# Kernel optimization log

Hardware: AMD Instinct MI355X
Metric: run time of the kernel (lower is better)

## Reference

```python
import jax, jax.numpy as jnp
import numpy as np

B, M, T, D, V = 16, 4096, 4, 256, 40000
HOPS, NLAYER, CONV_MAX = 3, 3, 512
PAD = 1  # PAD_token: embedding row zeroed (padding_idx)


def setup_inputs() -> dict:
    key = jax.random.key(0)
    ks = jax.random.split(key, 10)
    story = jax.random.randint(ks[0], (B, M, T), 0, V)
    conv_len = jax.random.randint(ks[1], (B,), 1, CONV_MAX)
    kb_len = jax.random.randint(ks[2], (B,), 0, M - CONV_MAX)
    query = jax.random.normal(ks[3], (B, 1, D), jnp.float32)
    history_outputs = jax.random.normal(ks[4], (B, CONV_MAX, D), jnp.float32)
    query_vector = jax.random.normal(ks[5], (B, D), jnp.float32)
    global_pointer = jax.random.uniform(ks[6], (B, M), jnp.float32)
    # hop+1 embedding tables, N(0, 0.1), padding row zeroed
    C_emb = jax.random.normal(ks[7], (HOPS + 1, V, D), jnp.float32) * 0.1
    C_emb = C_emb.at[:, PAD, :].set(0.0)
    Tg_w = jax.random.normal(ks[8], (HOPS + 1, D, D), jnp.float32) * 0.05
    Tg_b = jnp.zeros((HOPS + 1, D), jnp.float32)
    FW_w = jax.random.normal(ks[9], (D, D), jnp.float32) * 0.05
    FW_b = jnp.zeros((D,), jnp.float32)
    return dict(story=story, kb_len=kb_len, conv_len=conv_len, query=query,
                history_outputs=history_outputs, query_vector=query_vector,
                global_pointer=global_pointer, C_emb=C_emb, Tg_w=Tg_w,
                Tg_b=Tg_b, FW_w=FW_w, FW_b=FW_b)


def _add_lm(mem, kb_len, conv_len, hist):
    # mem: [B,M,D]; add hist[b, 0:conv_len[b]] into mem[b, kb_len[b]:kb_len[b]+conv_len[b]]
    j = jnp.arange(mem.shape[1])[None, :]                       # [1,M]
    start = kb_len[:, None]
    mask = (j >= start) & (j < start + conv_len[:, None])       # [B,M]
    idx = jnp.clip(j - start, 0, hist.shape[1] - 1)             # [B,M]
    gathered = jnp.take_along_axis(hist, idx[..., None], axis=1)  # [B,M,D]
    return mem + jnp.where(mask[..., None], gathered, 0.0)


def _embed(table, story, kb_len, conv_len, hist):
    # bag-of-words over the mem-token axis, then LM-embedding add
    e = jnp.sum(table[story], axis=2)                           # [B,M,D]
    return _add_lm(e, kb_len, conv_len, hist)


def reference(story, kb_len, conv_len, query, history_outputs, query_vector,
              global_pointer, C_emb, Tg_w, Tg_b, FW_w, FW_b):
    # ---- load_memory (eval mode: dropout is identity; ablationH/G = False) ----
    q = query[:, 0, :]                                          # [B,D]
    last_u = None
    m_story = None
    for layer in range(NLAYER):
        iq = q
        if layer > 0:
            g = jax.nn.sigmoid(iq @ Tg_w[0].T + Tg_b[0])
            iq = last_u[0] * g + iq * (1.0 - g)
        u = [iq]
        m_story = []
        embC = None
        for hop in range(HOPS):
            embA = _embed(C_emb[hop], story, kb_len, conv_len, history_outputs)
            logit = jnp.einsum('bmd,bd->bm', embA, u[-1])
            prob = jax.nn.softmax(logit, axis=1)
            embC = _embed(C_emb[hop + 1], story, kb_len, conv_len, history_outputs)
            o_k = jnp.einsum('bm,bmd->bd', prob, embC)
            u_k = u[-1] + o_k
            if layer > 0:
                g = jax.nn.sigmoid(u_k @ Tg_w[hop + 1].T + Tg_b[hop + 1])
                u_k = last_u[hop + 1] * g + u_k * (1.0 - g)
            u.append(u_k)
            m_story.append(embA)
        m_story.append(embC)
        last_u = u
        q = jax.nn.relu(u[-1] @ FW_w.T + FW_b)
    # ---- forward (decoder-side read over last layer's memories) ----
    uf = query_vector
    psoft = None
    logits = None
    for hop in range(HOPS):
        mA = m_story[hop] * global_pointer[:, :, None]
        logits = jnp.einsum('bmd,bd->bm', mA, uf)
        psoft = jax.nn.softmax(logits, axis=1)
        mC = m_story[hop + 1] * global_pointer[:, :, None]
        uf = uf + jnp.einsum('bm,bmd->bd', psoft, mC)
    return (psoft, logits, uf, m_story[-1])
```

## Files before the change

kernel.cpp:

```cpp
#include <hip/hip_runtime.h>
#include <math.h>

#define Bdim 16
#define Mdim 4096
#define Tdim 4
#define Ddim 256
#define Vdim 40000
#define CONVMAX 512

__global__ void embed_kernel(const int* __restrict__ story, const int* __restrict__ kb_len,
                             const int* __restrict__ conv_len, const float* __restrict__ hist,
                             const float* __restrict__ C_emb, const float* __restrict__ qv,
                             const float* __restrict__ gp,
                             float* __restrict__ e1, float* __restrict__ e2,
                             float* __restrict__ e3, float* __restrict__ logits0) {
    int bid = blockIdx.x;
    int k   = bid / (Bdim * (Mdim / 4));
    int rem = bid % (Bdim * (Mdim / 4));
    int b   = rem / (Mdim / 4);
    int mc  = rem % (Mdim / 4);
    int tid = threadIdx.x;
    int mi  = tid >> 6;
    int lane = tid & 63;
    int m   = mc * 4 + mi;
    int d4  = lane * 4;

    const int* st = story + ((size_t)b * Mdim + m) * Tdim;
    const float* tab = C_emb + (size_t)k * Vdim * Ddim;
    float4 acc = make_float4(0.f, 0.f, 0.f, 0.f);
#pragma unroll
    for (int t = 0; t < Tdim; ++t) {
        int row = st[t];
        const float4 v = *(const float4*)(tab + (size_t)row * Ddim + d4);
        acc.x += v.x; acc.y += v.y; acc.z += v.z; acc.w += v.w;
    }
    int kb = kb_len[b], cl = conv_len[b];
    if (m >= kb && m < kb + cl) {
        const float4 h = *(const float4*)(hist + ((size_t)b * CONVMAX + (m - kb)) * Ddim + d4);
        acc.x += h.x; acc.y += h.y; acc.z += h.z; acc.w += h.w;
    }
    if (k == 0) {
        const float4 uv = *(const float4*)(qv + (size_t)b * Ddim + d4);
        float p = acc.x * uv.x + acc.y * uv.y + acc.z * uv.z + acc.w * uv.w;
#pragma unroll
        for (int off = 32; off > 0; off >>= 1) p += __shfl_xor(p, off, 64);
        if (lane == 0) {
            size_t row = (size_t)b * Mdim + m;
            logits0[row] = p * gp[row];
        }
    } else {
        float* outp = (k == 1) ? e1 : (k == 2) ? e2 : e3;
        *(float4*)(outp + ((size_t)b * Mdim + m) * Ddim + d4) = acc;
    }
}

__global__ void logit_kernel(const float* __restrict__ emb, const float* __restrict__ u,
                             const float* __restrict__ gp, float* __restrict__ logits) {
    int tid = threadIdx.x;
    int mi = tid >> 6, lane = tid & 63;
    int row = blockIdx.x * 4 + mi;
    int b = row >> 12;
    const float4 e  = *(const float4*)(emb + (size_t)row * Ddim + lane * 4);
    const float4 uv = *(const float4*)(u + (size_t)b * Ddim + lane * 4);
    float p = e.x * uv.x + e.y * uv.y + e.z * uv.z + e.w * uv.w;
#pragma unroll
    for (int off = 32; off > 0; off >>= 1) p += __shfl_xor(p, off, 64);
    if (lane == 0) logits[row] = p * gp[row];
}

__global__ void stats_kernel(const float* __restrict__ logits, float* __restrict__ maxv,
                             float* __restrict__ rsum) {
    int b = blockIdx.x, tid = threadIdx.x;
    __shared__ float sh[256];
    const float* lg = logits + (size_t)b * Mdim;
    float mx = -INFINITY;
    for (int i = tid; i < Mdim; i += 256) mx = fmaxf(mx, lg[i]);
    sh[tid] = mx; __syncthreads();
    for (int s = 128; s > 0; s >>= 1) { if (tid < s) sh[tid] = fmaxf(sh[tid], sh[tid + s]); __syncthreads(); }
    float bm = sh[0]; __syncthreads();
    float sm = 0.f;
    for (int i = tid; i < Mdim; i += 256) sm += expf(lg[i] - bm);
    sh[tid] = sm; __syncthreads();
    for (int s = 128; s > 0; s >>= 1) { if (tid < s) sh[tid] += sh[tid + s]; __syncthreads(); }
    if (tid == 0) { maxv[b] = bm; rsum[b] = 1.0f / sh[0]; }
}

#define MT 128
__global__ void attend_kernel(const float* __restrict__ embC, const float* __restrict__ logits,
                              const float* __restrict__ maxv, const float* __restrict__ rsum,
                              const float* __restrict__ gp, float* __restrict__ acc_out) {
    int bid = blockIdx.x;
    int b  = bid / (Mdim / MT);
    int m0 = (bid % (Mdim / MT)) * MT;
    int tid = threadIdx.x;
    int wave = tid >> 6, lane = tid & 63;
    __shared__ float prob[MT];
    __shared__ float4 red[4][64];
    if (tid < MT) {
        size_t row = (size_t)b * Mdim + m0 + tid;
        prob[tid] = expf(logits[row] - maxv[b]) * rsum[b] * gp[row];
    }
    __syncthreads();
    float4 acc = make_float4(0.f, 0.f, 0.f, 0.f);
    const float4* base = (const float4*)(embC + ((size_t)b * Mdim + m0) * Ddim) + lane;
#pragma unroll 4
    for (int mm = wave; mm < MT; mm += 4) {
        float p = prob[mm];
        float4 v = base[(size_t)mm * (Ddim / 4)];
        acc.x += p * v.x; acc.y += p * v.y; acc.z += p * v.z; acc.w += p * v.w;
    }
    red[wave][lane] = acc;
    __syncthreads();
    if (wave == 0) {
        float4 a0 = red[0][lane], a1 = red[1][lane], a2 = red[2][lane], a3 = red[3][lane];
        float* dst = acc_out + (size_t)b * Ddim + lane * 4;
        atomicAdd(dst + 0, a0.x + a1.x + a2.x + a3.x);
        atomicAdd(dst + 1, a0.y + a1.y + a2.y + a3.y);
        atomicAdd(dst + 2, a0.z + a1.z + a2.z + a3.z);
        atomicAdd(dst + 3, a0.w + a1.w + a2.w + a3.w);
    }
}

__global__ void copy_kernel(const float* __restrict__ src, float* __restrict__ dst) {
    int b = blockIdx.x, i = threadIdx.x;
    dst[(size_t)b * Ddim + i] = src[(size_t)b * Ddim + i];
}

__global__ void psoft_kernel(const float* __restrict__ logits, const float* __restrict__ maxv,
                             const float* __restrict__ rsum, float* __restrict__ psoft) {
    int row = blockIdx.x * 256 + threadIdx.x;
    int b = row >> 12;
    psoft[row] = expf(logits[row] - maxv[b]) * rsum[b];
}

extern "C" void kernel_launch(void* const* d_in, const int* in_sizes, int n_in,
                              void* d_out, int out_size, void* d_ws, size_t ws_size,
                              hipStream_t stream) {
    const int*   story        = (const int*)d_in[0];
    const int*   kb_len       = (const int*)d_in[1];
    const int*   conv_len     = (const int*)d_in[2];
    const float* hist         = (const float*)d_in[4];
    const float* query_vector = (const float*)d_in[5];
    const float* gp           = (const float*)d_in[6];
    const float* C_emb        = (const float*)d_in[7];

    float* out        = (float*)d_out;
    float* out_psoft  = out;
    float* out_logits = out + (size_t)Bdim * Mdim;
    float* out_uf     = out + 2 * (size_t)Bdim * Mdim;
    float* out_m      = out + 2 * (size_t)Bdim * Mdim + (size_t)Bdim * Ddim;

    const size_t EMB = (size_t)Bdim * Mdim * Ddim;
    float* ws = (float*)d_ws;
    float* emb1   = ws;
    float* emb2   = ws + EMB;
    float* logits = ws + 2 * EMB;
    float* maxv   = logits + (size_t)Bdim * Mdim;
    float* rsum   = maxv + Bdim;

    embed_kernel<<<4 * Bdim * (Mdim / 4), 256, 0, stream>>>(
        story, kb_len, conv_len, hist, C_emb, query_vector, gp, emb1, emb2, out_m, logits);

    copy_kernel<<<Bdim, Ddim, 0, stream>>>(query_vector, out_uf);

    stats_kernel<<<Bdim, 256, 0, stream>>>(logits, maxv, rsum);
    attend_kernel<<<Bdim * (Mdim / MT), 256, 0, stream>>>(emb1, logits, maxv, rsum, gp, out_uf);

    logit_kernel<<<Bdim * Mdim / 4, 256, 0, stream>>>(emb1, out_uf, gp, logits);
    stats_kernel<<<Bdim, 256, 0, stream>>>(logits, maxv, rsum);
    attend_kernel<<<Bdim * (Mdim / MT), 256, 0, stream>>>(emb2, logits, maxv, rsum, gp, out_uf);

    logit_kernel<<<Bdim * Mdim / 4, 256, 0, stream>>>(emb2, out_uf, gp, out_logits);
    stats_kernel<<<Bdim, 256, 0, stream>>>(out_logits, maxv, rsum);
    attend_kernel<<<Bdim * (Mdim / MT), 256, 0, stream>>>(out_m, out_logits, maxv, rsum, gp, out_uf);
    psoft_kernel<<<Bdim * Mdim / 256, 256, 0, stream>>>(out_logits, maxv, rsum, out_psoft);
}
```

Measured before the change: 480.3 us.

## Recompute bag-of-words embeddings on the fly instead of materializing intermediate memories

Drops the two large workspace embedding tensors (each B*M*D floats). The logit and attention kernels now gather and sum the table rows directly from story indices every time they need them. The final attention pass also writes the last memory and the softmax output, which replaces the separate psoft and copy kernels. This trades large streaming writes and reads of intermediates for repeated random gathers from the tables. Those gathers may hit L2/MALL cache but add extra gather traffic and latency.

```diff
diff --git a/kernel.cpp b/kernel.cpp
--- a/kernel.cpp
+++ b/kernel.cpp
@@ -7,65 +7,43 @@
 #define Ddim 256
 #define Vdim 40000
 #define CONVMAX 512
+#define MT 64
 
-__global__ void embed_kernel(const int* __restrict__ story, const int* __restrict__ kb_len,
-                             const int* __restrict__ conv_len, const float* __restrict__ hist,
-                             const float* __restrict__ C_emb, const float* __restrict__ qv,
-                             const float* __restrict__ gp,
-                             float* __restrict__ e1, float* __restrict__ e2,
-                             float* __restrict__ e3, float* __restrict__ logits0) {
-    int bid = blockIdx.x;
-    int k   = bid / (Bdim * (Mdim / 4));
-    int rem = bid % (Bdim * (Mdim / 4));
-    int b   = rem / (Mdim / 4);
-    int mc  = rem % (Mdim / 4);
-    int tid = threadIdx.x;
-    int mi  = tid >> 6;
-    int lane = tid & 63;
-    int m   = mc * 4 + mi;
-    int d4  = lane * 4;
+__global__ void init_kernel(const float* __restrict__ qv, float* __restrict__ uf) {
+    int b = blockIdx.x, i = threadIdx.x;
+    uf[(size_t)b * Ddim + i] = qv[(size_t)b * Ddim + i];
+}
 
-    const int* st = story + ((size_t)b * Mdim + m) * Tdim;
-    const float* tab = C_emb + (size_t)k * Vdim * Ddim;
-    float4 acc = make_float4(0.f, 0.f, 0.f, 0.f);
+__global__ void qk_kernel(const int* __restrict__ story, const int* __restrict__ kb_len,
+                          const int* __restrict__ conv_len, const float* __restrict__ hist,
+                          const float* __restrict__ tab, const float* __restrict__ uf,
+                          const float* __restrict__ gp, float* __restrict__ logits) {
+    int tid = threadIdx.x, wave = tid >> 6, lane = tid & 63;
+    int row0 = blockIdx.x * 16 + wave * 4;
+    int b = row0 >> 12;
+    int d4 = lane * 4;
+    const float4 uv = *(const float4*)(uf + (size_t)b * Ddim + d4);
+    int kb = kb_len[b], cl = conv_len[b];
 #pragma unroll
-    for (int t = 0; t < Tdim; ++t) {
-        int row = st[t];
-        const float4 v = *(const float4*)(tab + (size_t)row * Ddim + d4);
-        acc.x += v.x; acc.y += v.y; acc.z += v.z; acc.w += v.w;
-    }
-    int kb = kb_len[b], cl = conv_len[b];
-    if (m >= kb && m < kb + cl) {
-        const float4 h = *(const float4*)(hist + ((size_t)b * CONVMAX + (m - kb)) * Ddim + d4);
-        acc.x += h.x; acc.y += h.y; acc.z += h.z; acc.w += h.w;
-    }
-    if (k == 0) {
-        const float4 uv = *(const float4*)(qv + (size_t)b * Ddim + d4);
+    for (int r = 0; r < 4; ++r) {
+        int row = row0 + r;
+        int m = row & (Mdim - 1);
+        const int* st = story + (size_t)row * Tdim;
+        float4 acc = make_float4(0.f, 0.f, 0.f, 0.f);
+#pragma unroll
+        for (int t = 0; t < Tdim; ++t) {
+            const float4 v = *(const float4*)(tab + (size_t)st[t] * Ddim + d4);
+            acc.x += v.x; acc.y += v.y; acc.z += v.z; acc.w += v.w;
+        }
+        if (m >= kb && m < kb + cl) {
+            const float4 h = *(const float4*)(hist + ((size_t)b * CONVMAX + (m - kb)) * Ddim + d4);
+            acc.x += h.x; acc.y += h.y; acc.z += h.z; acc.w += h.w;
+        }
         float p = acc.x * uv.x + acc.y * uv.y + acc.z * uv.z + acc.w * uv.w;
 #pragma unroll
         for (int off = 32; off > 0; off >>= 1) p += __shfl_xor(p, off, 64);
-        if (lane == 0) {
-            size_t row = (size_t)b * Mdim + m;
-            logits0[row] = p * gp[row];
-        }
-    } else {
-        float* outp = (k == 1) ? e1 : (k == 2) ? e2 : e3;
-        *(float4*)(outp + ((size_t)b * Mdim + m) * Ddim + d4) = acc;
+        if (lane == 0) logits[row] = p * gp[row];
     }
-}
-
-__global__ void logit_kernel(const float* __restrict__ emb, const float* __restrict__ u,
-                             const float* __restrict__ gp, float* __restrict__ logits) {
-    int tid = threadIdx.x;
-    int mi = tid >> 6, lane = tid & 63;
-    int row = blockIdx.x * 4 + mi;
-    int b = row >> 12;
-    const float4 e  = *(const float4*)(emb + (size_t)row * Ddim + lane * 4);
-    const float4 uv = *(const float4*)(u + (size_t)b * Ddim + lane * 4);
-    float p = e.x * uv.x + e.y * uv.y + e.z * uv.z + e.w * uv.w;
-#pragma unroll
-    for (int off = 32; off > 0; off >>= 1) p += __shfl_xor(p, off, 64);
-    if (lane == 0) logits[row] = p * gp[row];
 }
 
 __global__ void stats_kernel(const float* __restrict__ logits, float* __restrict__ maxv,
@@ -85,52 +63,58 @@
     if (tid == 0) { maxv[b] = bm; rsum[b] = 1.0f / sh[0]; }
 }
 
-#define MT 128
-__global__ void attend_kernel(const float* __restrict__ embC, const float* __restrict__ logits,
-                              const float* __restrict__ maxv, const float* __restrict__ rsum,
-                              const float* __restrict__ gp, float* __restrict__ acc_out) {
+__global__ void att_kernel(const int* __restrict__ story, const int* __restrict__ kb_len,
+                           const int* __restrict__ conv_len, const float* __restrict__ hist,
+                           const float* __restrict__ tab, const float* __restrict__ logits,
+                           const float* __restrict__ maxv, const float* __restrict__ rsum,
+                           const float* __restrict__ gp,
+                           float* __restrict__ uf_acc, float* __restrict__ out_m,
+                           float* __restrict__ out_psoft) {
     int bid = blockIdx.x;
     int b  = bid / (Mdim / MT);
     int m0 = (bid % (Mdim / MT)) * MT;
-    int tid = threadIdx.x;
-    int wave = tid >> 6, lane = tid & 63;
+    int tid = threadIdx.x, wave = tid >> 6, lane = tid & 63;
+    int d4 = lane * 4;
     __shared__ float prob[MT];
     __shared__ float4 red[4][64];
     if (tid < MT) {
         size_t row = (size_t)b * Mdim + m0 + tid;
-        prob[tid] = expf(logits[row] - maxv[b]) * rsum[b] * gp[row];
+        float pn = expf(logits[row] - maxv[b]) * rsum[b];
+        if (out_psoft) out_psoft[row] = pn;
+        prob[tid] = pn * gp[row];
     }
     __syncthreads();
+    int kb = kb_len[b], cl = conv_len[b];
     float4 acc = make_float4(0.f, 0.f, 0.f, 0.f);
-    const float4* base = (const float4*)(embC + ((size_t)b * Mdim + m0) * Ddim) + lane;
 #pragma unroll 4
     for (int mm = wave; mm < MT; mm += 4) {
+        int m = m0 + mm;
+        size_t row = (size_t)b * Mdim + m;
+        const int* st = story + row * Tdim;
+        float4 v = make_float4(0.f, 0.f, 0.f, 0.f);
+#pragma unroll
+        for (int t = 0; t < Tdim; ++t) {
+            const float4 w = *(const float4*)(tab + (size_t)st[t] * Ddim + d4);
+            v.x += w.x; v.y += w.y; v.z += w.z; v.w += w.w;
+        }
+        if (m >= kb && m < kb + cl) {
+            const float4 h = *(const float4*)(hist + ((size_t)b * CONVMAX + (m - kb)) * Ddim + d4);
+            v.x += h.x; v.y += h.y; v.z += h.z; v.w += h.w;
+        }
+        if (out_m) *(float4*)(out_m + row * Ddim + d4) = v;
         float p = prob[mm];
-        float4 v = base[(size_t)mm * (Ddim / 4)];
         acc.x += p * v.x; acc.y += p * v.y; acc.z += p * v.z; acc.w += p * v.w;
     }
     red[wave][lane] = acc;
     __syncthreads();
     if (wave == 0) {
         float4 a0 = red[0][lane], a1 = red[1][lane], a2 = red[2][lane], a3 = red[3][lane];
-        float* dst = acc_out + (size_t)b * Ddim + lane * 4;
+        float* dst = uf_acc + (size_t)b * Ddim + d4;
         atomicAdd(dst + 0, a0.x + a1.x + a2.x + a3.x);
         atomicAdd(dst + 1, a0.y + a1.y + a2.y + a3.y);
         atomicAdd(dst + 2, a0.z + a1.z + a2.z + a3.z);
         atomicAdd(dst + 3, a0.w + a1.w + a2.w + a3.w);
     }
-}
-
-__global__ void copy_kernel(const float* __restrict__ src, float* __restrict__ dst) {
-    int b = blockIdx.x, i = threadIdx.x;
-    dst[(size_t)b * Ddim + i] = src[(size_t)b * Ddim + i];
-}
-
-__global__ void psoft_kernel(const float* __restrict__ logits, const float* __restrict__ maxv,
-                             const float* __restrict__ rsum, float* __restrict__ psoft) {
-    int row = blockIdx.x * 256 + threadIdx.x;
-    int b = row >> 12;
-    psoft[row] = expf(logits[row] - maxv[b]) * rsum[b];
 }
 
 extern "C" void kernel_launch(void* const* d_in, const int* in_sizes, int n_in,
@@ -150,28 +134,38 @@
     float* out_uf     = out + 2 * (size_t)Bdim * Mdim;
     float* out_m      = out + 2 * (size_t)Bdim * Mdim + (size_t)Bdim * Ddim;
 
-    const size_t EMB = (size_t)Bdim * Mdim * Ddim;
     float* ws = (float*)d_ws;
-    float* emb1   = ws;
-    float* emb2   = ws + EMB;
-    float* logits = ws + 2 * EMB;
+    float* logits = ws;
     float* maxv   = logits + (size_t)Bdim * Mdim;
     float* rsum   = maxv + Bdim;
 
-    embed_kernel<<<4 * Bdim * (Mdim / 4), 256, 0, stream>>>(
-        story, kb_len, conv_len, hist, C_emb, query_vector, gp, emb1, emb2, out_m, logits);
+    const size_t TAB = (size_t)Vdim * Ddim;
+    const float* tab0 = C_emb;
+    const float* tab1 = C_emb + TAB;
+    const float* tab2 = C_emb + 2 * TAB;
+    const float* tab3 = C_emb + 3 * TAB;
 
-    copy_kernel<<<Bdim, Ddim, 0, stream>>>(query_vector, out_uf);
+    const int QK_GRID  = Bdim * Mdim / 16;
+    const int ATT_GRID = Bdim * (Mdim / MT);
 
+    init_kernel<<<Bdim, Ddim, 0, stream>>>(query_vector, out_uf);
+
+    qk_kernel<<<QK_GRID, 256, 0, stream>>>(story, kb_len, conv_len, hist,
+                                           tab0, query_vector, gp, logits);
     stats_kernel<<<Bdim, 256, 0, stream>>>(logits, maxv, rsum);
-    attend_kernel<<<Bdim * (Mdim / MT), 256, 0, stream>>>(emb1, logits, maxv, rsum, gp, out_uf);
-
-    logit_kernel<<<Bdim * Mdim / 4, 256, 0, stream>>>(emb1, out_uf, gp, logits);
+    att_kernel<<<ATT_GRID, 256, 0, stream>>>(story, kb_len, conv_len, hist,
+                                             tab1, logits, maxv, rsum, gp,
+                                             out_uf, nullptr, nullptr);
+    qk_kernel<<<QK_GRID, 256, 0, stream>>>(story, kb_len, conv_len, hist,
+                                           tab1, out_uf, gp, logits);
     stats_kernel<<<Bdim, 256, 0, stream>>>(logits, maxv, rsum);
-    attend_kernel<<<Bdim * (Mdim / MT), 256, 0, stream>>>(emb2, logits, maxv, rsum, gp, out_uf);
-
-    logit_kernel<<<Bdim * Mdim / 4, 256, 0, stream>>>(emb2, out_uf, gp, out_logits);
+    att_kernel<<<ATT_GRID, 256, 0, stream>>>(story, kb_len, conv_len, hist,
+                                             tab2, logits, maxv, rsum, gp,
+                                             out_uf, nullptr, nullptr);
+    qk_kernel<<<QK_GRID, 256, 0, stream>>>(story, kb_len, conv_len, hist,
+                                           tab2, out_uf, gp, out_logits);
     stats_kernel<<<Bdim, 256, 0, stream>>>(out_logits, maxv, rsum);
-    attend_kernel<<<Bdim * (Mdim / MT), 256, 0, stream>>>(out_m, out_logits, maxv, rsum, gp, out_uf);
-    psoft_kernel<<<Bdim * Mdim / 256, 256, 0, stream>>>(out_logits, maxv, rsum, out_psoft);
+    att_kernel<<<ATT_GRID, 256, 0, stream>>>(story, kb_len, conv_len, hist,
+                                             tab3, out_logits, maxv, rsum, gp,
+                                             out_uf, out_m, out_psoft);
 }
```

After: 490.4 us. 2.1% more time.
